# Optimization experiments

Hardware: AMD Instinct MI355X
Metric: run time of the kernel (lower is better)

The kernel has to match this reference:

```python
import jax, jax.numpy as jnp
import numpy as np

EMBED_DIM = 768
NUM_HEADS = 12
HEAD_DIM = EMBED_DIM // NUM_HEADS
ROPE_BASE = 10000.0


def setup_inputs() -> dict:
    key = jax.random.key(0)
    k1, k2, k3, k4, k5 = jax.random.split(key, 5)
    B, S, E = 1, 4096, EMBED_DIM
    x = jax.random.normal(k1, (B, S, E), dtype=jnp.float32)
    # causal mask: 1 where attend allowed, 0 elsewhere
    mask = jnp.tril(jnp.ones((S, S), dtype=jnp.int32))
    scale = 1.0 / np.sqrt(E)
    Wqkv = jax.random.normal(k2, (E, 3 * E), dtype=jnp.float32) * scale
    bqkv = jax.random.normal(k3, (3 * E,), dtype=jnp.float32) * 0.01
    Wout = jax.random.normal(k4, (E, E), dtype=jnp.float32) * scale
    bout = jax.random.normal(k5, (E,), dtype=jnp.float32) * 0.01
    return {"x": x, "mask": mask, "Wqkv": Wqkv, "bqkv": bqkv, "Wout": Wout, "bout": bout}


def _rope_cos_sin(seq_len, dtype):
    inv_freq = 1.0 / (ROPE_BASE ** (jnp.arange(0, HEAD_DIM, 2, dtype=jnp.float32) / HEAD_DIM))
    t = jnp.arange(seq_len, dtype=dtype)
    freqs = jnp.outer(t, inv_freq.astype(dtype))  # [S, Dh/2]
    emb = jnp.concatenate([freqs, freqs], axis=-1)  # [S, Dh]
    return jnp.cos(emb), jnp.sin(emb)


def _rotate_half(u):
    u1, u2 = jnp.split(u, 2, axis=-1)
    return jnp.concatenate([-u2, u1], axis=-1)


def reference(x, mask, Wqkv, bqkv, Wout, bout):
    B, S, E = x.shape
    H, Dh = NUM_HEADS, HEAD_DIM
    qkv = x @ Wqkv + bqkv  # [B, S, 3E]
    qkv = qkv.reshape(B, S, 3, H, Dh).transpose(2, 0, 3, 1, 4)  # [3, B, H, S, Dh]
    Q, K, V = qkv[0], qkv[1], qkv[2]
    # RoPE
    cos, sin = _rope_cos_sin(S, x.dtype)  # [S, Dh]
    cos = cos[None, None]
    sin = sin[None, None]
    Q = Q * cos + _rotate_half(Q) * sin
    K = K * cos + _rotate_half(K) * sin
    scores = jnp.einsum('bhsd,bhtd->bhst', Q, K) / jnp.sqrt(jnp.asarray(Dh, x.dtype))
    scores = jnp.where(mask[None, None] == 0, jnp.finfo(x.dtype).min, scores)
    attn = jax.nn.softmax(scores, axis=-1)  # dropout p=0 (eval) -> identity
    out = jnp.einsum('bhst,bhtd->bhsd', attn, V)  # [B, H, S, Dh]
    out = out.transpose(0, 2, 1, 3).reshape(B, S, E)
    return out @ Wout + bout
```

## Files before the change

### kernel.cpp

```cpp
#include <hip/hip_runtime.h>

typedef unsigned short u16;
typedef unsigned int   u32;
using short8 = __attribute__((ext_vector_type(8))) short;
using f32x4  = __attribute__((ext_vector_type(4))) float;
using f32x16 = __attribute__((ext_vector_type(16))) float;
using u32x4  = __attribute__((ext_vector_type(4))) unsigned int;

#define S_LEN 4096
#define EMB   768
#define NH    12
#define DH    64

#define QSCALE 0.18033688011112042f

__device__ __forceinline__ u16 f2bf(float f) {
  unsigned int u = __builtin_bit_cast(unsigned int, f);
  u += 0x7fffu + ((u >> 16) & 1u);
  return (u16)(u >> 16);
}

__device__ __forceinline__ u32 cvtpk(float lo, float hi) {
  u32 r;
  asm("v_cvt_pk_bf16_f32 %0, %1, %2" : "=v"(r) : "v"(lo), "v"(hi));
  return r;
}

__device__ __forceinline__ short8 pack8(const float* p) {
  f32x4 x0 = *(const f32x4*)p;
  f32x4 x1 = *(const f32x4*)(p + 4);
  u32x4 r = { cvtpk(x0[0], x0[1]), cvtpk(x0[2], x0[3]),
              cvtpk(x1[0], x1[1]), cvtpk(x1[2], x1[3]) };
  return __builtin_bit_cast(short8, r);
}

__device__ __forceinline__ void gld16(const void* g, void* l) {
  __builtin_amdgcn_global_load_lds(
      (const __attribute__((address_space(1))) void*)g,
      (__attribute__((address_space(3))) void*)l, 16, 0, 0);
}

__device__ __forceinline__ float pr_max(float v) {
  return fmaxf(v, __shfl_xor(v, 32));
}
__device__ __forceinline__ float pr_add(float v) {
  return v + __shfl_xor(v, 32);
}

__device__ __forceinline__ float fexp2(float x) {
#if __has_builtin(__builtin_amdgcn_exp2f)
  return __builtin_amdgcn_exp2f(x);
#else
  return exp2f(x);
#endif
}

__device__ __forceinline__ f32x4 mfma16(short8 a, short8 b, f32x4 c) {
  return __builtin_amdgcn_mfma_f32_16x16x32_bf16(a, b, c, 0, 0, 0);
}
__device__ __forceinline__ f32x16 mfma32(short8 a, short8 b, f32x16 c) {
  return __builtin_amdgcn_mfma_f32_32x32x16_bf16(a, b, c, 0, 0, 0);
}

__device__ __forceinline__ short8 pack_frag(u32 w0, u32 w1, u32 w2, u32 w3, bool hi) {
  u32 x0 = (u32)__shfl_xor((int)w0, 32), x1 = (u32)__shfl_xor((int)w1, 32);
  u32 x2 = (u32)__shfl_xor((int)w2, 32), x3 = (u32)__shfl_xor((int)w3, 32);
  u32x4 f = { hi ? x2 : w0, hi ? x3 : w1, hi ? w2 : x0, hi ? w3 : x1 };
  return __builtin_bit_cast(short8, f);
}


__device__ __forceinline__ void transpose_tile(const float* __restrict__ w,
                                               u16* __restrict__ wt,
                                               int rows, int cols,
                                               int kb, int nb,
                                               float (*tile)[33]) {
  int tx = threadIdx.x & 31, ty = threadIdx.x >> 5;
#pragma unroll
  for (int j = 0; j < 4; j++)
    tile[ty + 8 * j][tx] = w[(size_t)(kb + ty + 8 * j) * cols + nb + tx];
  __syncthreads();
#pragma unroll
  for (int j = 0; j < 4; j++)
    wt[(size_t)(nb + ty + 8 * j) * rows + kb + tx] = f2bf(tile[tx][ty + 8 * j]);
}

__global__ __launch_bounds__(256) void k_prep(const float* __restrict__ x,
                                              u16* __restrict__ xb,
                                              const float* __restrict__ Wqkv,
                                              u16* __restrict__ wqkvt,
                                              const float* __restrict__ Wout,
                                              u16* __restrict__ woutt) {
  __shared__ float tile[32][33];
  int b = blockIdx.x;
  if (b < 1536) {
    int i = (b * 256 + threadIdx.x) * 8;
    *(short8*)(xb + i) = pack8(x + i);
  } else if (b < 3264) {
    int bb = b - 1536;
    transpose_tile(Wqkv, wqkvt, EMB, 3 * EMB, (bb % 24) * 32, (bb / 24) * 32, tile);
  } else {
    int bb = b - 3264;
    transpose_tile(Wout, woutt, EMB, EMB, (bb % 24) * 32, (bb / 24) * 32, tile);
  }
}

__global__ __launch_bounds__(256) void k_qkv(const u16* __restrict__ A,
                                             const u16* __restrict__ Bt,
                                             const float* __restrict__ bias,
                                             u16* __restrict__ Qb,
                                             u16* __restrict__ Kb,
                                             u16* __restrict__ Vt) {
  __shared__ u16 AsL[128 * 32];
  __shared__ u16 BsL[128 * 32];
  int t = threadIdx.x;
  int w = t >> 6, lane = t & 63, g = lane >> 4, c = lane & 15;
  int wr = w >> 1, wc = w & 1;
  int bm = blockIdx.x * 128, bn = blockIdx.y * 128;

  f32x4 acc[4][4];
#pragma unroll
  for (int m = 0; m < 4; m++)
#pragma unroll
    for (int n = 0; n < 4; n++) acc[m][n] = (f32x4){0.f, 0.f, 0.f, 0.f};

  int r0 = t >> 2, cc0 = (t & 3) * 8;
  int r1 = (256 + t) >> 2;
  const u16* ga0 = A  + (size_t)(bm + r0) * EMB + cc0;
  const u16* ga1 = A  + (size_t)(bm + r1) * EMB + cc0;
  const u16* gb0 = Bt + (size_t)(bn + r0) * EMB + cc0;
  const u16* gb1 = Bt + (size_t)(bn + r1) * EMB + cc0;

  for (int bk = 0; bk < EMB; bk += 32) {
    __syncthreads();
    gld16(ga0 + bk, &AsL[(size_t)t * 8]);
    gld16(ga1 + bk, &AsL[(size_t)(256 + t) * 8]);
    gld16(gb0 + bk, &BsL[(size_t)t * 8]);
    gld16(gb1 + bk, &BsL[(size_t)(256 + t) * 8]);
    __syncthreads();
    short8 af[4], bf[4];
#pragma unroll
    for (int m = 0; m < 4; m++) af[m] = *(const short8*)&AsL[(wr * 64 + m * 16 + c) * 32 + g * 8];
#pragma unroll
    for (int n = 0; n < 4; n++) bf[n] = *(const short8*)&BsL[(wc * 64 + n * 16 + c) * 32 + g * 8];
#pragma unroll
    for (int m = 0; m < 4; m++)
#pragma unroll
      for (int n = 0; n < 4; n++) acc[m][n] = mfma16(af[m], bf[n], acc[m][n]);
  }

  int colbase = bn + wc * 64;
  int sec = colbase / EMB;
  int hh  = (colbase % EMB) / DH;
  float qs = (sec == 0) ? QSCALE : 1.0f;
  float invf[2];
#pragma unroll
  for (int n = 0; n < 2; n++) {
    int d1 = n * 16 + c;
    invf[n] = exp2f(-(float)d1 * (13.287712379549449f / 32.0f));
  }
#pragma unroll
  for (int m = 0; m < 4; m++) {
    int rowb = bm + wr * 64 + m * 16 + 4 * g;
#pragma unroll
    for (int e = 0; e < 4; e++) {
      int srw = rowb + e;
      float v[4];
#pragma unroll
      for (int n = 0; n < 4; n++) v[n] = acc[m][n][e] + bias[colbase + n * 16 + c];
      if (sec == 2) {
#pragma unroll
        for (int n = 0; n < 4; n++)
          Vt[(size_t)(hh * DH + n * 16 + c) * S_LEN + srw] = f2bf(v[n]);
      } else {
        u16* dst = (sec == 0) ? Qb : Kb;
        size_t base = ((size_t)hh * S_LEN + srw) * DH;
#pragma unroll
        for (int n = 0; n < 2; n++) {
          int d1 = n * 16 + c;
          float ang = (float)srw * invf[n];
          float sn, cs;
          sincosf(ang, &sn, &cs);
          float o1 = (v[n] * cs - v[n + 2] * sn) * qs;
          float o2 = (v[n + 2] * cs + v[n] * sn) * qs;
          dst[base + d1]      = f2bf(o1);
          dst[base + d1 + 32] = f2bf(o2);
        }
      }
    }
  }
}


template<bool MASKED>
__device__ __forceinline__ void attn_tile(int kv0, int qi, int half,
    const u16* __restrict__ Kh, const u16* __restrict__ Vh,
    short8 qf0, short8 qf1, short8 qf2, short8 qf3,
    f32x16& acc0, f32x16& acc1, float& m, float& l) {
  const u16* kp = Kh + (size_t)(kv0 + qi) * DH + half * 8;
  short8 k0 = *(const short8*)(kp);
  short8 k1 = *(const short8*)(kp + 16);
  short8 k2 = *(const short8*)(kp + 32);
  short8 k3 = *(const short8*)(kp + 48);
  __builtin_amdgcn_s_setprio(1);
  f32x16 sc = {0,0,0,0,0,0,0,0,0,0,0,0,0,0,0,0};
  sc = mfma32(k0, qf0, sc);
  sc = mfma32(k1, qf1, sc);
  sc = mfma32(k2, qf2, sc);
  sc = mfma32(k3, qf3, sc);
  __builtin_amdgcn_s_setprio(0);
  const u16* vp = Vh + (size_t)qi * S_LEN + kv0 + half * 8;
  short8 v00 = *(const short8*)(vp);
  short8 v01 = *(const short8*)(vp + 16);
  short8 v10 = *(const short8*)(vp + (size_t)32 * S_LEN);
  short8 v11 = *(const short8*)(vp + (size_t)32 * S_LEN + 16);
  if (MASKED) {
#pragma unroll
    for (int i = 0; i < 16; i++) {
      int kl = (i & 3) + 8 * (i >> 2) + 4 * half;
      if (kl > qi) sc[i] = -1e30f;
    }
  }
  float t0 = fmaxf(fmaxf(sc[0], sc[1]), fmaxf(sc[2], sc[3]));
  float t1 = fmaxf(fmaxf(sc[4], sc[5]), fmaxf(sc[6], sc[7]));
  float t2 = fmaxf(fmaxf(sc[8], sc[9]), fmaxf(sc[10], sc[11]));
  float t3 = fmaxf(fmaxf(sc[12], sc[13]), fmaxf(sc[14], sc[15]));
  float rmax = pr_max(fmaxf(fmaxf(t0, t1), fmaxf(t2, t3)));
  if (__any(rmax > m + 8.0f)) {
    float mn = fmaxf(m, rmax);
    float f = fexp2(m - mn);
    m = mn; l *= f;
#pragma unroll
    for (int i = 0; i < 16; i++) { acc0[i] *= f; acc1[i] *= f; }
  }
  f32x16 p;
#pragma unroll
  for (int i = 0; i < 16; i++) p[i] = fexp2(sc[i] - m);
  l += ((p[0] + p[1]) + (p[2] + p[3])) + ((p[4] + p[5]) + (p[6] + p[7]))
     + ((p[8] + p[9]) + (p[10] + p[11])) + ((p[12] + p[13]) + (p[14] + p[15]));
  bool hi = (half != 0);
  short8 pa0 = pack_frag(cvtpk(p[0], p[1]),   cvtpk(p[2], p[3]),
                         cvtpk(p[4], p[5]),   cvtpk(p[6], p[7]), hi);
  short8 pa1 = pack_frag(cvtpk(p[8], p[9]),   cvtpk(p[10], p[11]),
                         cvtpk(p[12], p[13]), cvtpk(p[14], p[15]), hi);
  __builtin_amdgcn_s_setprio(1);
  acc0 = mfma32(v00, pa0, acc0);
  acc0 = mfma32(v01, pa1, acc0);
  acc1 = mfma32(v10, pa0, acc1);
  acc1 = mfma32(v11, pa1, acc1);
  __builtin_amdgcn_s_setprio(0);
}

__device__ __forceinline__ void attn_tile2(int kv0, int qi, int half,
    const u16* __restrict__ Kh, const u16* __restrict__ Vh,
    short8 qf0, short8 qf1, short8 qf2, short8 qf3,
    f32x16& acc0, f32x16& acc1, float& m, float& l) {
  const u16* kpa = Kh + (size_t)(kv0 + qi) * DH + half * 8;
  const u16* kpb = kpa + (size_t)32 * DH;
  short8 ka0 = *(const short8*)(kpa);
  short8 ka1 = *(const short8*)(kpa + 16);
  short8 ka2 = *(const short8*)(kpa + 32);
  short8 ka3 = *(const short8*)(kpa + 48);
  short8 kb0 = *(const short8*)(kpb);
  short8 kb1 = *(const short8*)(kpb + 16);
  short8 kb2 = *(const short8*)(kpb + 32);
  short8 kb3 = *(const short8*)(kpb + 48);
  __builtin_amdgcn_s_setprio(1);
  f32x16 sa = {0,0,0,0,0,0,0,0,0,0,0,0,0,0,0,0};
  f32x16 sb = {0,0,0,0,0,0,0,0,0,0,0,0,0,0,0,0};
  sa = mfma32(ka0, qf0, sa);
  sb = mfma32(kb0, qf0, sb);
  sa = mfma32(ka1, qf1, sa);
  sb = mfma32(kb1, qf1, sb);
  sa = mfma32(ka2, qf2, sa);
  sb = mfma32(kb2, qf2, sb);
  sa = mfma32(ka3, qf3, sa);
  sb = mfma32(kb3, qf3, sb);
  __builtin_amdgcn_s_setprio(0);
  const u16* vpa = Vh + (size_t)qi * S_LEN + kv0 + half * 8;
  const u16* vpb = vpa + 32;
  short8 va00 = *(const short8*)(vpa);
  short8 va01 = *(const short8*)(vpa + 16);
  short8 va10 = *(const short8*)(vpa + (size_t)32 * S_LEN);
  short8 va11 = *(const short8*)(vpa + (size_t)32 * S_LEN + 16);
  short8 vb00 = *(const short8*)(vpb);
  short8 vb01 = *(const short8*)(vpb + 16);
  short8 vb10 = *(const short8*)(vpb + (size_t)32 * S_LEN);
  short8 vb11 = *(const short8*)(vpb + (size_t)32 * S_LEN + 16);
  float t0 = fmaxf(fmaxf(sa[0], sa[1]), fmaxf(sa[2], sa[3]));
  float t1 = fmaxf(fmaxf(sa[4], sa[5]), fmaxf(sa[6], sa[7]));
  float t2 = fmaxf(fmaxf(sa[8], sa[9]), fmaxf(sa[10], sa[11]));
  float t3 = fmaxf(fmaxf(sa[12], sa[13]), fmaxf(sa[14], sa[15]));
  float u0 = fmaxf(fmaxf(sb[0], sb[1]), fmaxf(sb[2], sb[3]));
  float u1 = fmaxf(fmaxf(sb[4], sb[5]), fmaxf(sb[6], sb[7]));
  float u2 = fmaxf(fmaxf(sb[8], sb[9]), fmaxf(sb[10], sb[11]));
  float u3 = fmaxf(fmaxf(sb[12], sb[13]), fmaxf(sb[14], sb[15]));
  float rmax = pr_max(fmaxf(fmaxf(fmaxf(t0, t1), fmaxf(t2, t3)),
                            fmaxf(fmaxf(u0, u1), fmaxf(u2, u3))));
  if (__any(rmax > m + 8.0f)) {
    float mn = fmaxf(m, rmax);
    float f = fexp2(m - mn);
    m = mn; l *= f;
#pragma unroll
    for (int i = 0; i < 16; i++) { acc0[i] *= f; acc1[i] *= f; }
  }
  f32x16 pa, pb;
#pragma unroll
  for (int i = 0; i < 16; i++) pa[i] = fexp2(sa[i] - m);
#pragma unroll
  for (int i = 0; i < 16; i++) pb[i] = fexp2(sb[i] - m);
  float la = ((pa[0] + pa[1]) + (pa[2] + pa[3])) + ((pa[4] + pa[5]) + (pa[6] + pa[7]))
           + ((pa[8] + pa[9]) + (pa[10] + pa[11])) + ((pa[12] + pa[13]) + (pa[14] + pa[15]));
  float lb = ((pb[0] + pb[1]) + (pb[2] + pb[3])) + ((pb[4] + pb[5]) + (pb[6] + pb[7]))
           + ((pb[8] + pb[9]) + (pb[10] + pb[11])) + ((pb[12] + pb[13]) + (pb[14] + pb[15]));
  l += la + lb;
  bool hi = (half != 0);
  short8 fa0 = pack_frag(cvtpk(pa[0], pa[1]),   cvtpk(pa[2], pa[3]),
                         cvtpk(pa[4], pa[5]),   cvtpk(pa[6], pa[7]), hi);
  short8 fa1 = pack_frag(cvtpk(pa[8], pa[9]),   cvtpk(pa[10], pa[11]),
                         cvtpk(pa[12], pa[13]), cvtpk(pa[14], pa[15]), hi);
  short8 fb0 = pack_frag(cvtpk(pb[0], pb[1]),   cvtpk(pb[2], pb[3]),
                         cvtpk(pb[4], pb[5]),   cvtpk(pb[6], pb[7]), hi);
  short8 fb1 = pack_frag(cvtpk(pb[8], pb[9]),   cvtpk(pb[10], pb[11]),
                         cvtpk(pb[12], pb[13]), cvtpk(pb[14], pb[15]), hi);
  __builtin_amdgcn_s_setprio(1);
  acc0 = mfma32(va00, fa0, acc0);
  acc1 = mfma32(va10, fa0, acc1);
  acc0 = mfma32(va01, fa1, acc0);
  acc1 = mfma32(va11, fa1, acc1);
  acc0 = mfma32(vb00, fb0, acc0);
  acc1 = mfma32(vb10, fb0, acc1);
  acc0 = mfma32(vb01, fb1, acc0);
  acc1 = mfma32(vb11, fb1, acc1);
  __builtin_amdgcn_s_setprio(0);
}

__global__ __launch_bounds__(256, 3) void k_attn(const u16* __restrict__ Q,
                                                 const u16* __restrict__ K,
                                                 const u16* __restrict__ Vt,
                                                 u16* __restrict__ O) {
  __shared__ float Lacc[3][64][33];
  __shared__ float Lml[2][3][32];

  int t = threadIdx.x;
  int w = t >> 6, lane = t & 63;
  int qi = lane & 31, half = lane >> 5;
  int b = blockIdx.x;
  int h = b % NH;
  int qb = 127 - b / NH;

  const u16* Qh = Q  + (size_t)h * S_LEN * DH;
  const u16* Kh = K  + (size_t)h * S_LEN * DH;
  const u16* Vh = Vt + (size_t)h * DH * S_LEN;

  const u16* qp = Qh + (size_t)(qb * 32 + qi) * DH + half * 8;
  short8 qf0 = *(const short8*)(qp);
  short8 qf1 = *(const short8*)(qp + 16);
  short8 qf2 = *(const short8*)(qp + 32);
  short8 qf3 = *(const short8*)(qp + 48);

  f32x16 acc0 = {0,0,0,0,0,0,0,0,0,0,0,0,0,0,0,0};
  f32x16 acc1 = {0,0,0,0,0,0,0,0,0,0,0,0,0,0,0,0};
  float m = -1e30f, l = 0.f;

  int nt = qb + 1;
  int ck = (nt + 3) >> 2;
  int start = w * ck;
  int end   = min(start + ck, nt);
  int endu  = min(end, nt - 1);
  int tt = start;
#pragma unroll 1
  for (; tt + 1 < endu; tt += 2)
    attn_tile2(tt * 32, qi, half, Kh, Vh, qf0, qf1, qf2, qf3, acc0, acc1, m, l);
  for (; tt < endu; tt++)
    attn_tile<false>(tt * 32, qi, half, Kh, Vh, qf0, qf1, qf2, qf3, acc0, acc1, m, l);
  if (start < nt && end == nt)
    attn_tile<true>((nt - 1) * 32, qi, half, Kh, Vh, qf0, qf1, qf2, qf3, acc0, acc1, m, l);

  float l2 = pr_add(l);
  if (w > 0) {
#pragma unroll
    for (int i = 0; i < 16; i++) {
      Lacc[w - 1][lane][i]      = acc0[i];
      Lacc[w - 1][lane][16 + i] = acc1[i];
    }
    if (half == 0) { Lml[0][w - 1][qi] = m; Lml[1][w - 1][qi] = l2; }
  }
  __syncthreads();
  if (w == 0) {
    float mw[3], lw[3];
    float M = m;
#pragma unroll
    for (int j = 0; j < 3; j++) { mw[j] = Lml[0][j][qi]; lw[j] = Lml[1][j][qi]; M = fmaxf(M, mw[j]); }
    float f0 = fexp2(m - M);
    float ltot = l2 * f0;
#pragma unroll
    for (int i = 0; i < 16; i++) { acc0[i] *= f0; acc1[i] *= f0; }
#pragma unroll
    for (int j = 0; j < 3; j++) {
      float fj = fexp2(mw[j] - M);
      ltot += lw[j] * fj;
#pragma unroll
      for (int i = 0; i < 16; i++) {
        acc0[i] += fj * Lacc[j][lane][i];
        acc1[i] += fj * Lacc[j][lane][16 + i];
      }
    }
    float rl = 1.0f / ltot;
    u16* orow = O + (size_t)(qb * 32 + qi) * EMB + h * DH;
#pragma unroll
    for (int i = 0; i < 16; i += 2) {
      int dl = (i & 3) + 8 * (i >> 2) + 4 * half;
      u32 wa = cvtpk(acc0[i] * rl, acc0[i + 1] * rl);
      u32 wb = cvtpk(acc1[i] * rl, acc1[i + 1] * rl);
      *(u32*)(orow + dl)      = wa;
      *(u32*)(orow + 32 + dl) = wb;
    }
  }
}

__global__ __launch_bounds__(256) void k_out(const u16* __restrict__ A,
                                             const u16* __restrict__ Bt,
                                             const float* __restrict__ bias,
                                             float* __restrict__ out) {
  __shared__ u16 AsL[128 * 32];
  __shared__ u16 BsL[64 * 32];
  int t = threadIdx.x;
  int w = t >> 6, lane = t & 63, g = lane >> 4, c = lane & 15;
  int bm = blockIdx.x * 128, bn = blockIdx.y * 64;

  f32x4 acc[2][4];
#pragma unroll
  for (int m = 0; m < 2; m++)
#pragma unroll
    for (int n = 0; n < 4; n++) acc[m][n] = (f32x4){0.f, 0.f, 0.f, 0.f};

  int r0 = t >> 2, cc0 = (t & 3) * 8;
  int r1 = (256 + t) >> 2;
  const u16* ga0 = A  + (size_t)(bm + r0) * EMB + cc0;
  const u16* ga1 = A  + (size_t)(bm + r1) * EMB + cc0;
  const u16* gb0 = Bt + (size_t)(bn + r0) * EMB + cc0;

  for (int bk = 0; bk < EMB; bk += 32) {
    __syncthreads();
    gld16(ga0 + bk, &AsL[(size_t)t * 8]);
    gld16(ga1 + bk, &AsL[(size_t)(256 + t) * 8]);
    gld16(gb0 + bk, &BsL[(size_t)t * 8]);
    __syncthreads();
    short8 af[2], bf[4];
#pragma unroll
    for (int m = 0; m < 2; m++) af[m] = *(const short8*)&AsL[(w * 32 + m * 16 + c) * 32 + g * 8];
#pragma unroll
    for (int n = 0; n < 4; n++) bf[n] = *(const short8*)&BsL[(n * 16 + c) * 32 + g * 8];
#pragma unroll
    for (int m = 0; m < 2; m++)
#pragma unroll
      for (int n = 0; n < 4; n++) acc[m][n] = mfma16(af[m], bf[n], acc[m][n]);
  }
#pragma unroll
  for (int m = 0; m < 2; m++) {
    int rowb = bm + w * 32 + m * 16 + 4 * g;
#pragma unroll
    for (int e = 0; e < 4; e++) {
      int srw = rowb + e;
#pragma unroll
      for (int n = 0; n < 4; n++) {
        int col = bn + n * 16 + c;
        out[(size_t)srw * EMB + col] = acc[m][n][e] + bias[col];
      }
    }
  }
}


extern "C" void kernel_launch(void* const* d_in, const int* in_sizes, int n_in,
                              void* d_out, int out_size, void* d_ws, size_t ws_size,
                              hipStream_t stream) {
  const float* x    = (const float*)d_in[0];
  const float* Wqkv = (const float*)d_in[2];
  const float* bqkv = (const float*)d_in[3];
  const float* Wout = (const float*)d_in[4];
  const float* bout = (const float*)d_in[5];
  float* out = (float*)d_out;

  char* ws = (char*)d_ws;
  u16* xb     = (u16*)(ws);
  u16* wqkvt  = (u16*)(ws + 6291456);
  u16* woutt  = (u16*)(ws + 9830400);
  u16* Qb     = (u16*)(ws + 11010048);
  u16* Kb     = (u16*)(ws + 17301504);
  u16* Vtb    = (u16*)(ws + 23592960);
  u16* Ob     = (u16*)(ws + 29884416);

  k_prep<<<3840, 256, 0, stream>>>(x, xb, Wqkv, wqkvt, Wout, woutt);
  k_qkv<<<dim3(32, 18), 256, 0, stream>>>(xb, wqkvt, bqkv, Qb, Kb, Vtb);
  k_attn<<<NH * 128, 256, 0, stream>>>(Qb, Kb, Vtb, Ob);
  k_out<<<dim3(32, 12), 256, 0, stream>>>(Ob, woutt, bout, out);
}
```

Before: 152.6 us.

## Split attention over KV chunks with LDS-staged K/V tiles and separate merge kernel

Adds a split-KV attention kernel where each block handles 128 query rows (four waves) over one quarter of the causal key range. K and V tiles are double-buffered through shared memory so the four waves share each load, and partial accumulators plus max/sum values are written to workspace. A new merge kernel then combines the four partials per query block. The old in-kernel pairwise tile path is removed and the old kernel is kept only as a fallback when the workspace is too small. The aim is more K/V reuse and better load balance, at the cost of a large fp32 partial buffer round-trip, an extra launch, and per-tile barriers. Waves whose rows are fully masked for a tile skip it but still wait at the barrier.

```diff
diff --git a/kernel.cpp b/kernel.cpp
--- a/kernel.cpp
+++ b/kernel.cpp
@@ -192,6 +192,181 @@
 }
 
 
+__device__ __forceinline__ f32x16 qk4(short8 k0, short8 k1, short8 k2, short8 k3,
+                                      short8 q0, short8 q1, short8 q2, short8 q3) {
+  f32x16 sc = {0,0,0,0,0,0,0,0,0,0,0,0,0,0,0,0};
+  __builtin_amdgcn_s_setprio(1);
+  sc = mfma32(k0, q0, sc);
+  sc = mfma32(k1, q1, sc);
+  sc = mfma32(k2, q2, sc);
+  sc = mfma32(k3, q3, sc);
+  __builtin_amdgcn_s_setprio(0);
+  return sc;
+}
+
+__device__ __forceinline__ void finish_set(f32x16 sc, bool masked, int qi, int half,
+    short8 v0, short8 v1, short8 v2, short8 v3,
+    f32x16& acc0, f32x16& acc1, float& m, float& l) {
+  if (masked) {
+#pragma unroll
+    for (int i = 0; i < 16; i++) {
+      int kl = (i & 3) + 8 * (i >> 2) + 4 * half;
+      if (kl > qi) sc[i] = -1e30f;
+    }
+  }
+  float t0 = fmaxf(fmaxf(sc[0], sc[1]), fmaxf(sc[2], sc[3]));
+  float t1 = fmaxf(fmaxf(sc[4], sc[5]), fmaxf(sc[6], sc[7]));
+  float t2 = fmaxf(fmaxf(sc[8], sc[9]), fmaxf(sc[10], sc[11]));
+  float t3 = fmaxf(fmaxf(sc[12], sc[13]), fmaxf(sc[14], sc[15]));
+  float rmax = pr_max(fmaxf(fmaxf(t0, t1), fmaxf(t2, t3)));
+  if (__any(rmax > m + 8.0f)) {
+    float mn = fmaxf(m, rmax);
+    float f = fexp2(m - mn);
+    m = mn; l *= f;
+#pragma unroll
+    for (int i = 0; i < 16; i++) { acc0[i] *= f; acc1[i] *= f; }
+  }
+  f32x16 p;
+#pragma unroll
+  for (int i = 0; i < 16; i++) p[i] = fexp2(sc[i] - m);
+  l += ((p[0] + p[1]) + (p[2] + p[3])) + ((p[4] + p[5]) + (p[6] + p[7]))
+     + ((p[8] + p[9]) + (p[10] + p[11])) + ((p[12] + p[13]) + (p[14] + p[15]));
+  bool hi = (half != 0);
+  short8 pa0 = pack_frag(cvtpk(p[0], p[1]),   cvtpk(p[2], p[3]),
+                         cvtpk(p[4], p[5]),   cvtpk(p[6], p[7]), hi);
+  short8 pa1 = pack_frag(cvtpk(p[8], p[9]),   cvtpk(p[10], p[11]),
+                         cvtpk(p[12], p[13]), cvtpk(p[14], p[15]), hi);
+  __builtin_amdgcn_s_setprio(1);
+  acc0 = mfma32(v0, pa0, acc0);
+  acc0 = mfma32(v1, pa1, acc0);
+  acc1 = mfma32(v2, pa0, acc1);
+  acc1 = mfma32(v3, pa1, acc1);
+  __builtin_amdgcn_s_setprio(0);
+}
+
+
+__global__ __launch_bounds__(256) void k_attn_split(const u16* __restrict__ Q,
+                                                    const u16* __restrict__ K,
+                                                    const u16* __restrict__ Vt,
+                                                    float* __restrict__ Pacc,
+                                                    float* __restrict__ Pml) {
+  __shared__ __align__(16) u16 KL[2][32][72];
+  __shared__ __align__(16) u16 VL[2][64][40];
+
+  int t = threadIdx.x;
+  int w = t >> 6, lane = t & 63;
+  int qi = lane & 31, half = lane >> 5;
+  int b = blockIdx.x;
+  int c = b & 3;
+  int hs = b >> 2;
+  int sb = 31 - hs / NH;
+  int h  = hs % NH;
+  int cs = sb + 1;
+  int t0 = c * cs, t1 = t0 + cs;
+  int diag = 4 * sb + w;
+
+  const u16* Kh = K  + (size_t)h * S_LEN * DH;
+  const u16* Vh = Vt + (size_t)h * DH * S_LEN;
+
+  int row  = w * 32 + qi;
+  int qrow = sb * 128 + row;
+  const u16* qp = Q + ((size_t)h * S_LEN + qrow) * DH + half * 8;
+  short8 qf0 = *(const short8*)(qp);
+  short8 qf1 = *(const short8*)(qp + 16);
+  short8 qf2 = *(const short8*)(qp + 32);
+  short8 qf3 = *(const short8*)(qp + 48);
+
+  int krow = t >> 3, kseg = t & 7;
+  int vrow = t >> 2, vseg = t & 3;
+  const u16* kg = Kh + (size_t)krow * DH + kseg * 8;
+  const u16* vg = Vh + (size_t)vrow * S_LEN + vseg * 8;
+
+  {
+    short8 ks = *(const short8*)(kg + (size_t)t0 * 32 * DH);
+    short8 vs = *(const short8*)(vg + t0 * 32);
+    *(short8*)&KL[0][krow][kseg * 8] = ks;
+    *(short8*)&VL[0][vrow][vseg * 8] = vs;
+  }
+  __syncthreads();
+
+  f32x16 acc0 = {0,0,0,0,0,0,0,0,0,0,0,0,0,0,0,0};
+  f32x16 acc1 = {0,0,0,0,0,0,0,0,0,0,0,0,0,0,0,0};
+  float m = -1e30f, l = 0.f;
+
+  int cur = 0;
+#pragma unroll 1
+  for (int tt = t0; tt < t1; tt++) {
+    bool more = (tt + 1 < t1);
+    short8 kn, vn;
+    if (more) {
+      kn = *(const short8*)(kg + (size_t)(tt + 1) * 32 * DH);
+      vn = *(const short8*)(vg + (tt + 1) * 32);
+    }
+    if (tt <= diag) {
+      short8 k0 = *(const short8*)&KL[cur][qi][half * 8];
+      short8 k1 = *(const short8*)&KL[cur][qi][half * 8 + 16];
+      short8 k2 = *(const short8*)&KL[cur][qi][half * 8 + 32];
+      short8 k3 = *(const short8*)&KL[cur][qi][half * 8 + 48];
+      f32x16 sc = qk4(k0, k1, k2, k3, qf0, qf1, qf2, qf3);
+      short8 v0 = *(const short8*)&VL[cur][qi][half * 8];
+      short8 v1 = *(const short8*)&VL[cur][qi][half * 8 + 16];
+      short8 v2 = *(const short8*)&VL[cur][32 + qi][half * 8];
+      short8 v3 = *(const short8*)&VL[cur][32 + qi][half * 8 + 16];
+      finish_set(sc, tt == diag, qi, half, v0, v1, v2, v3, acc0, acc1, m, l);
+    }
+    if (more) {
+      *(short8*)&KL[cur ^ 1][krow][kseg * 8] = kn;
+      *(short8*)&VL[cur ^ 1][vrow][vseg * 8] = vn;
+    }
+    __syncthreads();
+    cur ^= 1;
+  }
+
+  float l2 = pr_add(l);
+  int blk = (h * 32 + sb) * 4 + c;
+  float* pa = Pacc + ((size_t)blk * 128 + row) * 64;
+#pragma unroll
+  for (int i = 0; i < 16; i++) {
+    int dl = (i & 3) + 8 * (i >> 2) + 4 * half;
+    pa[dl]      = acc0[i];
+    pa[32 + dl] = acc1[i];
+  }
+  if (half == 0) {
+    Pml[(size_t)(blk * 2 + 0) * 128 + row] = m;
+    Pml[(size_t)(blk * 2 + 1) * 128 + row] = l2;
+  }
+}
+
+__global__ __launch_bounds__(256) void k_merge(const float* __restrict__ Pacc,
+                                               const float* __restrict__ Pml,
+                                               u16* __restrict__ O) {
+  int b = blockIdx.x;
+  int h = b % NH, sb = b / NH;
+  int blk0 = (h * 32 + sb) * 4;
+#pragma unroll 1
+  for (int e = threadIdx.x; e < 128 * 64; e += 256) {
+    int row = e >> 6, d = e & 63;
+    float mw[4], lw[4];
+    float M = -1e30f;
+#pragma unroll
+    for (int c = 0; c < 4; c++) {
+      mw[c] = Pml[(size_t)((blk0 + c) * 2 + 0) * 128 + row];
+      lw[c] = Pml[(size_t)((blk0 + c) * 2 + 1) * 128 + row];
+      M = fmaxf(M, mw[c]);
+    }
+    float ltot = 0.f, o = 0.f;
+#pragma unroll
+    for (int c = 0; c < 4; c++) {
+      float f = fexp2(mw[c] - M);
+      ltot += lw[c] * f;
+      o += f * Pacc[((size_t)(blk0 + c) * 128 + row) * 64 + d];
+    }
+    int qrow = sb * 128 + row;
+    O[(size_t)qrow * EMB + h * DH + d] = f2bf(o / ltot);
+  }
+}
+
+
 template<bool MASKED>
 __device__ __forceinline__ void attn_tile(int kv0, int qi, int half,
     const u16* __restrict__ Kh, const u16* __restrict__ Vh,
@@ -202,137 +377,13 @@
   short8 k1 = *(const short8*)(kp + 16);
   short8 k2 = *(const short8*)(kp + 32);
   short8 k3 = *(const short8*)(kp + 48);
-  __builtin_amdgcn_s_setprio(1);
-  f32x16 sc = {0,0,0,0,0,0,0,0,0,0,0,0,0,0,0,0};
-  sc = mfma32(k0, qf0, sc);
-  sc = mfma32(k1, qf1, sc);
-  sc = mfma32(k2, qf2, sc);
-  sc = mfma32(k3, qf3, sc);
-  __builtin_amdgcn_s_setprio(0);
+  f32x16 sc = qk4(k0, k1, k2, k3, qf0, qf1, qf2, qf3);
   const u16* vp = Vh + (size_t)qi * S_LEN + kv0 + half * 8;
-  short8 v00 = *(const short8*)(vp);
-  short8 v01 = *(const short8*)(vp + 16);
-  short8 v10 = *(const short8*)(vp + (size_t)32 * S_LEN);
-  short8 v11 = *(const short8*)(vp + (size_t)32 * S_LEN + 16);
-  if (MASKED) {
-#pragma unroll
-    for (int i = 0; i < 16; i++) {
-      int kl = (i & 3) + 8 * (i >> 2) + 4 * half;
-      if (kl > qi) sc[i] = -1e30f;
-    }
-  }
-  float t0 = fmaxf(fmaxf(sc[0], sc[1]), fmaxf(sc[2], sc[3]));
-  float t1 = fmaxf(fmaxf(sc[4], sc[5]), fmaxf(sc[6], sc[7]));
-  float t2 = fmaxf(fmaxf(sc[8], sc[9]), fmaxf(sc[10], sc[11]));
-  float t3 = fmaxf(fmaxf(sc[12], sc[13]), fmaxf(sc[14], sc[15]));
-  float rmax = pr_max(fmaxf(fmaxf(t0, t1), fmaxf(t2, t3)));
-  if (__any(rmax > m + 8.0f)) {
-    float mn = fmaxf(m, rmax);
-    float f = fexp2(m - mn);
-    m = mn; l *= f;
-#pragma unroll
-    for (int i = 0; i < 16; i++) { acc0[i] *= f; acc1[i] *= f; }
-  }
-  f32x16 p;
-#pragma unroll
-  for (int i = 0; i < 16; i++) p[i] = fexp2(sc[i] - m);
-  l += ((p[0] + p[1]) + (p[2] + p[3])) + ((p[4] + p[5]) + (p[6] + p[7]))
-     + ((p[8] + p[9]) + (p[10] + p[11])) + ((p[12] + p[13]) + (p[14] + p[15]));
-  bool hi = (half != 0);
-  short8 pa0 = pack_frag(cvtpk(p[0], p[1]),   cvtpk(p[2], p[3]),
-                         cvtpk(p[4], p[5]),   cvtpk(p[6], p[7]), hi);
-  short8 pa1 = pack_frag(cvtpk(p[8], p[9]),   cvtpk(p[10], p[11]),
-                         cvtpk(p[12], p[13]), cvtpk(p[14], p[15]), hi);
-  __builtin_amdgcn_s_setprio(1);
-  acc0 = mfma32(v00, pa0, acc0);
-  acc0 = mfma32(v01, pa1, acc0);
-  acc1 = mfma32(v10, pa0, acc1);
-  acc1 = mfma32(v11, pa1, acc1);
-  __builtin_amdgcn_s_setprio(0);
-}
-
-__device__ __forceinline__ void attn_tile2(int kv0, int qi, int half,
-    const u16* __restrict__ Kh, const u16* __restrict__ Vh,
-    short8 qf0, short8 qf1, short8 qf2, short8 qf3,
-    f32x16& acc0, f32x16& acc1, float& m, float& l) {
-  const u16* kpa = Kh + (size_t)(kv0 + qi) * DH + half * 8;
-  const u16* kpb = kpa + (size_t)32 * DH;
-  short8 ka0 = *(const short8*)(kpa);
-  short8 ka1 = *(const short8*)(kpa + 16);
-  short8 ka2 = *(const short8*)(kpa + 32);
-  short8 ka3 = *(const short8*)(kpa + 48);
-  short8 kb0 = *(const short8*)(kpb);
-  short8 kb1 = *(const short8*)(kpb + 16);
-  short8 kb2 = *(const short8*)(kpb + 32);
-  short8 kb3 = *(const short8*)(kpb + 48);
-  __builtin_amdgcn_s_setprio(1);
-  f32x16 sa = {0,0,0,0,0,0,0,0,0,0,0,0,0,0,0,0};
-  f32x16 sb = {0,0,0,0,0,0,0,0,0,0,0,0,0,0,0,0};
-  sa = mfma32(ka0, qf0, sa);
-  sb = mfma32(kb0, qf0, sb);
-  sa = mfma32(ka1, qf1, sa);
-  sb = mfma32(kb1, qf1, sb);
-  sa = mfma32(ka2, qf2, sa);
-  sb = mfma32(kb2, qf2, sb);
-  sa = mfma32(ka3, qf3, sa);
-  sb = mfma32(kb3, qf3, sb);
-  __builtin_amdgcn_s_setprio(0);
-  const u16* vpa = Vh + (size_t)qi * S_LEN + kv0 + half * 8;
-  const u16* vpb = vpa + 32;
-  short8 va00 = *(const short8*)(vpa);
-  short8 va01 = *(const short8*)(vpa + 16);
-  short8 va10 = *(const short8*)(vpa + (size_t)32 * S_LEN);
-  short8 va11 = *(const short8*)(vpa + (size_t)32 * S_LEN + 16);
-  short8 vb00 = *(const short8*)(vpb);
-  short8 vb01 = *(const short8*)(vpb + 16);
-  short8 vb10 = *(const short8*)(vpb + (size_t)32 * S_LEN);
-  short8 vb11 = *(const short8*)(vpb + (size_t)32 * S_LEN + 16);
-  float t0 = fmaxf(fmaxf(sa[0], sa[1]), fmaxf(sa[2], sa[3]));
-  float t1 = fmaxf(fmaxf(sa[4], sa[5]), fmaxf(sa[6], sa[7]));
-  float t2 = fmaxf(fmaxf(sa[8], sa[9]), fmaxf(sa[10], sa[11]));
-  float t3 = fmaxf(fmaxf(sa[12], sa[13]), fmaxf(sa[14], sa[15]));
-  float u0 = fmaxf(fmaxf(sb[0], sb[1]), fmaxf(sb[2], sb[3]));
-  float u1 = fmaxf(fmaxf(sb[4], sb[5]), fmaxf(sb[6], sb[7]));
-  float u2 = fmaxf(fmaxf(sb[8], sb[9]), fmaxf(sb[10], sb[11]));
-  float u3 = fmaxf(fmaxf(sb[12], sb[13]), fmaxf(sb[14], sb[15]));
-  float rmax = pr_max(fmaxf(fmaxf(fmaxf(t0, t1), fmaxf(t2, t3)),
-                            fmaxf(fmaxf(u0, u1), fmaxf(u2, u3))));
-  if (__any(rmax > m + 8.0f)) {
-    float mn = fmaxf(m, rmax);
-    float f = fexp2(m - mn);
-    m = mn; l *= f;
-#pragma unroll
-    for (int i = 0; i < 16; i++) { acc0[i] *= f; acc1[i] *= f; }
-  }
-  f32x16 pa, pb;
-#pragma unroll
-  for (int i = 0; i < 16; i++) pa[i] = fexp2(sa[i] - m);
-#pragma unroll
-  for (int i = 0; i < 16; i++) pb[i] = fexp2(sb[i] - m);
-  float la = ((pa[0] + pa[1]) + (pa[2] + pa[3])) + ((pa[4] + pa[5]) + (pa[6] + pa[7]))
-           + ((pa[8] + pa[9]) + (pa[10] + pa[11])) + ((pa[12] + pa[13]) + (pa[14] + pa[15]));
-  float lb = ((pb[0] + pb[1]) + (pb[2] + pb[3])) + ((pb[4] + pb[5]) + (pb[6] + pb[7]))
-           + ((pb[8] + pb[9]) + (pb[10] + pb[11])) + ((pb[12] + pb[13]) + (pb[14] + pb[15]));
-  l += la + lb;
-  bool hi = (half != 0);
-  short8 fa0 = pack_frag(cvtpk(pa[0], pa[1]),   cvtpk(pa[2], pa[3]),
-                         cvtpk(pa[4], pa[5]),   cvtpk(pa[6], pa[7]), hi);
-  short8 fa1 = pack_frag(cvtpk(pa[8], pa[9]),   cvtpk(pa[10], pa[11]),
-                         cvtpk(pa[12], pa[13]), cvtpk(pa[14], pa[15]), hi);
-  short8 fb0 = pack_frag(cvtpk(pb[0], pb[1]),   cvtpk(pb[2], pb[3]),
-                         cvtpk(pb[4], pb[5]),   cvtpk(pb[6], pb[7]), hi);
-  short8 fb1 = pack_frag(cvtpk(pb[8], pb[9]),   cvtpk(pb[10], pb[11]),
-                         cvtpk(pb[12], pb[13]), cvtpk(pb[14], pb[15]), hi);
-  __builtin_amdgcn_s_setprio(1);
-  acc0 = mfma32(va00, fa0, acc0);
-  acc1 = mfma32(va10, fa0, acc1);
-  acc0 = mfma32(va01, fa1, acc0);
-  acc1 = mfma32(va11, fa1, acc1);
-  acc0 = mfma32(vb00, fb0, acc0);
-  acc1 = mfma32(vb10, fb0, acc1);
-  acc0 = mfma32(vb01, fb1, acc0);
-  acc1 = mfma32(vb11, fb1, acc1);
-  __builtin_amdgcn_s_setprio(0);
+  short8 v0 = *(const short8*)(vp);
+  short8 v1 = *(const short8*)(vp + 16);
+  short8 v2 = *(const short8*)(vp + (size_t)32 * S_LEN);
+  short8 v3 = *(const short8*)(vp + (size_t)32 * S_LEN + 16);
+  finish_set(sc, MASKED, qi, half, v0, v1, v2, v3, acc0, acc1, m, l);
 }
 
 __global__ __launch_bounds__(256, 3) void k_attn(const u16* __restrict__ Q,
@@ -368,11 +419,8 @@
   int start = w * ck;
   int end   = min(start + ck, nt);
   int endu  = min(end, nt - 1);
-  int tt = start;
 #pragma unroll 1
-  for (; tt + 1 < endu; tt += 2)
-    attn_tile2(tt * 32, qi, half, Kh, Vh, qf0, qf1, qf2, qf3, acc0, acc1, m, l);
-  for (; tt < endu; tt++)
+  for (int tt = start; tt < endu; tt++)
     attn_tile<false>(tt * 32, qi, half, Kh, Vh, qf0, qf1, qf2, qf3, acc0, acc1, m, l);
   if (start < nt && end == nt)
     attn_tile<true>((nt - 1) * 32, qi, half, Kh, Vh, qf0, qf1, qf2, qf3, acc0, acc1, m, l);
@@ -491,9 +539,17 @@
   u16* Kb     = (u16*)(ws + 17301504);
   u16* Vtb    = (u16*)(ws + 23592960);
   u16* Ob     = (u16*)(ws + 29884416);
+  float* Pacc = (float*)(ws + 36175872);
+  float* Pml  = (float*)(ws + 86507520);
+  const size_t WS_NEEDED = 88080384;
 
   k_prep<<<3840, 256, 0, stream>>>(x, xb, Wqkv, wqkvt, Wout, woutt);
   k_qkv<<<dim3(32, 18), 256, 0, stream>>>(xb, wqkvt, bqkv, Qb, Kb, Vtb);
-  k_attn<<<NH * 128, 256, 0, stream>>>(Qb, Kb, Vtb, Ob);
+  if (ws_size >= WS_NEEDED) {
+    k_attn_split<<<1536, 256, 0, stream>>>(Qb, Kb, Vtb, Pacc, Pml);
+    k_merge<<<384, 256, 0, stream>>>(Pacc, Pml, Ob);
+  } else {
+    k_attn<<<NH * 128, 256, 0, stream>>>(Qb, Kb, Vtb, Ob);
+  }
   k_out<<<dim3(32, 12), 256, 0, stream>>>(Ob, woutt, bout, out);
 }
```

Result: no change. 153.3 us (+0.5%).
